# Kernel tuning notes

Hardware: AMD Instinct MI355X
Metric: run time of the kernel (lower is better)

The kernel has to match this reference:

```python
import jax, jax.numpy as jnp
import numpy as np

EMBED_DIM = 1024
NUM_HEADS = 16
HEAD_DIM = EMBED_DIM // NUM_HEADS


def setup_inputs() -> dict:
    key = jax.random.key(0)
    k_x, k_wqkv, k_bqkv, k_wo, k_bo = jax.random.split(key, 5)
    bound = 1.0 / np.sqrt(EMBED_DIM)
    x = jax.random.normal(k_x, (2, 2048, EMBED_DIM), dtype=jnp.float32)
    # torch Linear weight is [out, in]; store as [in, out] for x @ W
    W_qkv = jax.random.uniform(k_wqkv, (EMBED_DIM, 3 * EMBED_DIM), minval=-bound, maxval=bound, dtype=jnp.float32)
    b_qkv = jax.random.uniform(k_bqkv, (3 * EMBED_DIM,), minval=-bound, maxval=bound, dtype=jnp.float32)
    W_out = jax.random.uniform(k_wo, (EMBED_DIM, EMBED_DIM), minval=-bound, maxval=bound, dtype=jnp.float32)
    b_out = jax.random.uniform(k_bo, (EMBED_DIM,), minval=-bound, maxval=bound, dtype=jnp.float32)
    return {"x": x, "W_qkv": W_qkv, "b_qkv": b_qkv, "W_out": W_out, "b_out": b_out}


def reference(x, W_qkv, b_qkv, W_out, b_out):
    B, T, D = x.shape
    H, Hd = NUM_HEADS, HEAD_DIM
    qkv = x @ W_qkv + b_qkv                      # [B,T,3D]
    qkv = qkv.reshape(B, T, 3, H, Hd)
    q = qkv[:, :, 0].transpose(0, 2, 1, 3)       # [B,H,T,Hd]
    k = qkv[:, :, 1].transpose(0, 2, 1, 3)
    v = qkv[:, :, 2].transpose(0, 2, 1, 3)
    scores = jnp.einsum('bhqd,bhkd->bhqk', q, k) / jnp.sqrt(jnp.float32(Hd))
    attn = jax.nn.softmax(scores, axis=-1)       # [B,H,T,T]
    out = jnp.einsum('bhqk,bhkd->bhqd', attn, v) # [B,H,T,Hd]
    out = out.transpose(0, 2, 1, 3).reshape(B, T, D)
    return out @ W_out + b_out
```

## Files before the change

### kernel.cpp

```cpp
#include <hip/hip_runtime.h>
#include <hip/hip_bf16.h>

#define B_   2
#define T_   2048
#define D_   1024
#define H_   16
#define HD_  64
#define M_TOT (B_*T_)
#define N_QKV (3*D_)

typedef __attribute__((ext_vector_type(8))) short bf16x8;
typedef __attribute__((ext_vector_type(4))) float f32x4;
typedef __attribute__((ext_vector_type(16))) float f32x16;

static __device__ __forceinline__ short f2bf(float f) {
    union { __hip_bfloat16 h; short s; } u;
    u.h = __float2bfloat16(f);
    return u.s;
}
static __device__ __forceinline__ unsigned pack2(float a, float b) {
    return (unsigned)(unsigned short)f2bf(a) | ((unsigned)(unsigned short)f2bf(b) << 16);
}
static __device__ __forceinline__ float exp2_fast(float x) {
    return __builtin_amdgcn_exp2f(x);
}
static __device__ __forceinline__ f32x16 zero16() {
    f32x16 z;
    #pragma unroll
    for (int i = 0; i < 16; ++i) z[i] = 0.f;
    return z;
}
static __device__ __forceinline__ void gload16(const void* g, void* l) {
    __builtin_amdgcn_global_load_lds(
        (__attribute__((address_space(1))) unsigned int*)(unsigned long long)g,
        (__attribute__((address_space(3))) unsigned int*)l, 16, 0, 0);
}

__global__ __launch_bounds__(256) void convert_x(const float* __restrict__ x,
                                                 short* __restrict__ xb, int n8) {
    int i = blockIdx.x * blockDim.x + threadIdx.x;
    if (i >= n8) return;
    const float4* p = (const float4*)x + (size_t)i * 2;
    float4 a = p[0], b = p[1];
    bf16x8 o;
    o[0]=f2bf(a.x); o[1]=f2bf(a.y); o[2]=f2bf(a.z); o[3]=f2bf(a.w);
    o[4]=f2bf(b.x); o[5]=f2bf(b.y); o[6]=f2bf(b.z); o[7]=f2bf(b.w);
    *((bf16x8*)xb + i) = o;
}

__global__ __launch_bounds__(256) void transpose_convert(const float* __restrict__ in,
                                                         short* __restrict__ out,
                                                         int K, int N) {
    __shared__ short tile[64][65];
    int k0 = blockIdx.y * 64, n0 = blockIdx.x * 64;
    int t = threadIdx.x;
    #pragma unroll
    for (int i = 0; i < 16; ++i) {
        int idx = i * 256 + t;
        int r = idx >> 6, c = idx & 63;
        tile[r][c] = f2bf(in[(size_t)(k0 + r) * N + n0 + c]);
    }
    __syncthreads();
    #pragma unroll
    for (int i = 0; i < 16; ++i) {
        int idx = i * 256 + t;
        int r = idx >> 6, c = idx & 63;
        out[(size_t)(n0 + r) * K + k0 + c] = tile[c][r];
    }
}

#define QSC 0.18033688f
template<int BM, int BN, int MODE>
__global__ __launch_bounds__(256)
void gemm_dl(const short* __restrict__ A, const short* __restrict__ BT,
             const float* __restrict__ bias, int M, int N, int K,
             short* __restrict__ qo, short* __restrict__ ko,
             short* __restrict__ vo, float* __restrict__ fo) {
    constexpr int BUF = (BM + BN) * 64;
    constexpr int NL = (BM + BN) / 64;
    __shared__ char smem[3 * BUF];
    const int t = threadIdx.x, w = t >> 6, l = t & 63;
    const int qi_l = l & 15, hi_l = l >> 4;
    const int m0 = blockIdx.y * BM, n0 = blockIdx.x * BN;
    const int wr = w >> 1, wc = w & 1;
    constexpr int MI = BM / 32, NI = BN / 32;

    f32x4 acc[MI][NI];
    #pragma unroll
    for (int mi = 0; mi < MI; ++mi)
        #pragma unroll
        for (int ni = 0; ni < NI; ++ni)
            acc[mi][ni] = (f32x4){0.f, 0.f, 0.f, 0.f};

    const int lrow = l >> 2;
    const int lch  = ((l & 3) ^ (lrow & 3)) * 8;

    auto stage = [&](char* dst, int k0) {
        #pragma unroll
        for (int i = 0; i < BM / 64; ++i) {
            int rb = w * (BM / 4) + i * 16;
            gload16(A + (size_t)(m0 + rb + lrow) * K + k0 + lch, dst + rb * 64);
        }
        #pragma unroll
        for (int i = 0; i < BN / 64; ++i) {
            int rb = w * (BN / 4) + i * 16;
            gload16(BT + (size_t)(n0 + rb + lrow) * K + k0 + lch, dst + BM * 64 + rb * 64);
        }
    };

    const int nt = K / 32;
    stage(smem, 0);
    if (nt > 1) stage(smem + BUF, 32);
    for (int it = 0; it < nt; ++it) {
        if (it + 2 < nt) {
            stage(smem + ((it + 2) % 3) * BUF, (it + 2) * 32);
            if constexpr (NL == 4)      asm volatile("s_waitcnt vmcnt(8)" ::: "memory");
            else if constexpr (NL == 3) asm volatile("s_waitcnt vmcnt(6)" ::: "memory");
            else                        asm volatile("s_waitcnt vmcnt(0)" ::: "memory");
        } else if (it + 1 < nt) {
            if constexpr (NL == 4)      asm volatile("s_waitcnt vmcnt(4)" ::: "memory");
            else if constexpr (NL == 3) asm volatile("s_waitcnt vmcnt(3)" ::: "memory");
            else                        asm volatile("s_waitcnt vmcnt(0)" ::: "memory");
        } else {
            asm volatile("s_waitcnt vmcnt(0)" ::: "memory");
        }
        __builtin_amdgcn_s_barrier();

        char* sA = smem + (it % 3) * BUF;
        char* sB = sA + BM * 64;
        bf16x8 af[MI], bfr[NI];
        #pragma unroll
        for (int mi = 0; mi < MI; ++mi) {
            int row = wr * (BM / 2) + mi * 16 + qi_l;
            int ad = row * 64 + ((hi_l ^ (row & 3)) * 16);
            af[mi] = *(const bf16x8*)(sA + ad);
        }
        #pragma unroll
        for (int ni = 0; ni < NI; ++ni) {
            int row = wc * (BN / 2) + ni * 16 + qi_l;
            int ad = row * 64 + ((hi_l ^ (row & 3)) * 16);
            bfr[ni] = *(const bf16x8*)(sB + ad);
        }
        #pragma unroll
        for (int mi = 0; mi < MI; ++mi)
            #pragma unroll
            for (int ni = 0; ni < NI; ++ni)
                acc[mi][ni] = __builtin_amdgcn_mfma_f32_16x16x32_bf16(af[mi], bfr[ni], acc[mi][ni], 0, 0, 0);

        __builtin_amdgcn_s_barrier();
    }

    #pragma unroll
    for (int mi = 0; mi < MI; ++mi) {
        int rbase = m0 + wr * (BM / 2) + mi * 16 + 4 * hi_l;
        #pragma unroll
        for (int ni = 0; ni < NI; ++ni) {
            int n = n0 + wc * (BN / 2) + ni * 16 + qi_l;
            float bv = bias[n];
            #pragma unroll
            for (int r = 0; r < 4; ++r) {
                int mm = rbase + r;
                float c = acc[mi][ni][r] + bv;
                if (MODE == 0) {
                    int which = n >> 10, rest = n & 1023;
                    int h = rest >> 6, d = rest & 63;
                    int b = mm >> 11, tq = mm & 2047;
                    size_t bh = (size_t)(b * H_ + h);
                    if (which == 0)      qo[(bh * T_ + tq) * HD_ + d] = f2bf(c * QSC);
                    else if (which == 1) ko[(bh * T_ + tq) * HD_ + d] = f2bf(c);
                    else                 vo[(bh * HD_ + d) * T_ + tq] = f2bf(c);
                } else {
                    fo[(size_t)mm * N + n] = c;
                }
            }
        }
    }
}

__global__ __launch_bounds__(512)
void attn(const short* __restrict__ q, const short* __restrict__ k,
          const short* __restrict__ vt, short* __restrict__ ao) {
    __shared__ char smem[32768];

    const int t = threadIdx.x, w = t >> 6, l = t & 63;
    const int q32 = l & 31, hi2 = l >> 5;
    const int swz = (l & 7) << 4;
    const int bh = blockIdx.y;
    const int q0 = blockIdx.x * 256 + w * 32;

    const short* qptr = q + ((size_t)bh * T_ + q0) * HD_;
    const short* kbase = k + (size_t)bh * T_ * HD_;
    const short* vbase = vt + (size_t)bh * HD_ * T_;

    const int srow = w * 8 + (l >> 3);
    const int sch  = ((l & 7) ^ (l >> 3)) * 8;

    bf16x8 qa[4];
    #pragma unroll
    for (int kc = 0; kc < 4; ++kc)
        qa[kc] = *(const bf16x8*)(qptr + q32 * HD_ + kc * 16 + hi2 * 8);

    f32x16 o0 = zero16(), o1 = zero16();
    float m = -1e30f, lsum = 0.f;

    gload16(kbase + (size_t)srow * HD_ + sch, smem + srow * 128);
    gload16(vbase + (size_t)srow * T_ + sch,  smem + 8192 + srow * 128);
    __syncthreads();

    int cur = 0;
    for (int kb = 0; kb < T_; kb += 64) {
        char* sK = smem + cur * 16384;
        char* sV = sK + 8192;
        if (kb + 64 < T_) {
            char* nK = smem + (cur ^ 1) * 16384;
            gload16(kbase + (size_t)(kb + 64 + srow) * HD_ + sch, nK + srow * 128);
            gload16(vbase + (size_t)srow * T_ + (kb + 64) + sch,  nK + 8192 + srow * 128);
        }

        f32x16 s0 = zero16(), s1 = zero16();
        #pragma unroll
        for (int kc = 0; kc < 4; ++kc) {
            int off = (kc * 32 + hi2 * 16) ^ swz;
            bf16x8 kf0 = *(const bf16x8*)(sK + q32 * 128 + off);
            s0 = __builtin_amdgcn_mfma_f32_32x32x16_bf16(kf0, qa[kc], s0, 0, 0, 0);
            bf16x8 kf1 = *(const bf16x8*)(sK + (32 + q32) * 128 + off);
            s1 = __builtin_amdgcn_mfma_f32_32x32x16_bf16(kf1, qa[kc], s1, 0, 0, 0);
        }

        float a8[8];
        #pragma unroll
        for (int i = 0; i < 8; ++i)
            a8[i] = fmaxf(fmaxf(s0[i], s0[i + 8]), fmaxf(s1[i], s1[i + 8]));
        float b4_0 = fmaxf(a8[0], a8[1]), b4_1 = fmaxf(a8[2], a8[3]);
        float b4_2 = fmaxf(a8[4], a8[5]), b4_3 = fmaxf(a8[6], a8[7]);
        float tm = fmaxf(fmaxf(b4_0, b4_1), fmaxf(b4_2, b4_3));
        tm = fmaxf(tm, __shfl_xor(tm, 32));

        if (!__all(tm <= m + 8.f)) {
            float mnew = fmaxf(m, tm);
            float fsc = exp2_fast(m - mnew);
            lsum *= fsc;
            #pragma unroll
            for (int i = 0; i < 16; ++i) { o0[i] *= fsc; o1[i] *= fsc; }
            m = mnew;
        }

        #pragma unroll
        for (int i = 0; i < 16; ++i) {
            s0[i] = exp2_fast(s0[i] - m);
            s1[i] = exp2_fast(s1[i] - m);
        }
        float p8[8];
        #pragma unroll
        for (int i = 0; i < 8; ++i)
            p8[i] = (s0[i] + s0[i + 8]) + (s1[i] + s1[i + 8]);
        float psum = ((p8[0] + p8[1]) + (p8[2] + p8[3])) + ((p8[4] + p8[5]) + (p8[6] + p8[7]));
        psum += __shfl_xor(psum, 32);
        lsum += psum;

        unsigned pk0[8], pk1[8];
        #pragma unroll
        for (int p = 0; p < 8; ++p) {
            pk0[p] = pack2(s0[2 * p], s0[2 * p + 1]);
            pk1[p] = pack2(s1[2 * p], s1[2 * p + 1]);
        }

        #pragma unroll
        for (int c = 0; c < 4; ++c) {
            unsigned w0 = (c & 2) ? pk1[(c & 1) * 4 + 0] : pk0[(c & 1) * 4 + 0];
            unsigned w1 = (c & 2) ? pk1[(c & 1) * 4 + 1] : pk0[(c & 1) * 4 + 1];
            unsigned w2 = (c & 2) ? pk1[(c & 1) * 4 + 2] : pk0[(c & 1) * 4 + 2];
            unsigned w3 = (c & 2) ? pk1[(c & 1) * 4 + 3] : pk0[(c & 1) * 4 + 3];
            unsigned t0 = hi2 ? w0 : w2;
            unsigned t1 = hi2 ? w1 : w3;
            unsigned r0 = __shfl_xor(t0, 32);
            unsigned r1 = __shfl_xor(t1, 32);
            union { unsigned u[4]; bf16x8 v; } uf;
            uf.u[0] = hi2 ? r0 : w0;
            uf.u[1] = hi2 ? r1 : w1;
            uf.u[2] = hi2 ? w2 : r0;
            uf.u[3] = hi2 ? w3 : r1;
            bf16x8 pf = uf.v;

            int off = (c * 32 + hi2 * 16) ^ swz;
            bf16x8 vf0 = *(const bf16x8*)(sV + q32 * 128 + off);
            o0 = __builtin_amdgcn_mfma_f32_32x32x16_bf16(vf0, pf, o0, 0, 0, 0);
            bf16x8 vf1 = *(const bf16x8*)(sV + (32 + q32) * 128 + off);
            o1 = __builtin_amdgcn_mfma_f32_32x32x16_bf16(vf1, pf, o1, 0, 0, 0);
        }

        __syncthreads();
        cur ^= 1;
    }

    const float inv = 1.f / lsum;
    const int b = bh >> 4, h = bh & 15;
    const int tq = q0 + q32;
    unsigned* aou = (unsigned*)(ao + ((size_t)(b * T_ + tq)) * D_ + h * HD_);
    #pragma unroll
    for (int pr = 0; pr < 8; ++pr) {
        int d0 = 2 * (pr & 1) + 8 * (pr >> 1) + 4 * hi2;
        aou[d0 >> 1]        = pack2(o0[2 * pr] * inv, o0[2 * pr + 1] * inv);
        aou[(32 + d0) >> 1] = pack2(o1[2 * pr] * inv, o1[2 * pr + 1] * inv);
    }
}

extern "C" void kernel_launch(void* const* d_in, const int* in_sizes, int n_in,
                              void* d_out, int out_size, void* d_ws, size_t ws_size,
                              hipStream_t stream) {
    const float* x    = (const float*)d_in[0];
    const float* Wqkv = (const float*)d_in[1];
    const float* bqkv = (const float*)d_in[2];
    const float* Wout = (const float*)d_in[3];
    const float* bout = (const float*)d_in[4];
    float* out = (float*)d_out;

    char* ws = (char*)d_ws;
    short* xb  = (short*)(ws);
    short* WqT = (short*)(ws + ((size_t)8  << 20));
    short* WoT = (short*)(ws + ((size_t)14 << 20));
    short* qb  = (short*)(ws + ((size_t)16 << 20));
    short* kb  = (short*)(ws + ((size_t)24 << 20));
    short* vtb = (short*)(ws + ((size_t)32 << 20));
    short* aob = (short*)(ws + ((size_t)40 << 20));

    convert_x<<<(M_TOT * D_ / 8 + 255) / 256, 256, 0, stream>>>(x, xb, M_TOT * D_ / 8);
    transpose_convert<<<dim3(N_QKV / 64, D_ / 64), 256, 0, stream>>>(Wqkv, WqT, D_, N_QKV);
    transpose_convert<<<dim3(D_ / 64, D_ / 64), 256, 0, stream>>>(Wout, WoT, D_, D_);

    gemm_dl<128, 128, 0><<<dim3(N_QKV / 128, M_TOT / 128), 256, 0, stream>>>(
        xb, WqT, bqkv, M_TOT, N_QKV, D_, qb, kb, vtb, nullptr);

    attn<<<dim3(T_ / 256, B_ * H_), 512, 0, stream>>>(qb, kb, vtb, aob);

    gemm_dl<128, 64, 1><<<dim3(D_ / 64, M_TOT / 128), 256, 0, stream>>>(
        aob, WoT, bout, M_TOT, D_, D_, nullptr, nullptr, nullptr, out);
}
```

Baseline: 130.3 us.

## Split attention KV range in two and merge partials with combine kernel

```diff
diff --git a/kernel.cpp b/kernel.cpp
--- a/kernel.cpp
+++ b/kernel.cpp
@@ -17,6 +17,11 @@
     union { __hip_bfloat16 h; short s; } u;
     u.h = __float2bfloat16(f);
     return u.s;
+}
+static __device__ __forceinline__ float bf2f(short s) {
+    union { unsigned u; float f; } v;
+    v.u = ((unsigned)(unsigned short)s) << 16;
+    return v.f;
 }
 static __device__ __forceinline__ unsigned pack2(float a, float b) {
     return (unsigned)(unsigned short)f2bf(a) | ((unsigned)(unsigned short)f2bf(b) << 16);
@@ -179,14 +184,17 @@
 
 __global__ __launch_bounds__(512)
 void attn(const short* __restrict__ q, const short* __restrict__ k,
-          const short* __restrict__ vt, short* __restrict__ ao) {
+          const short* __restrict__ vt, short* __restrict__ pO,
+          float2* __restrict__ ml) {
     __shared__ char smem[32768];
 
     const int t = threadIdx.x, w = t >> 6, l = t & 63;
     const int q32 = l & 31, hi2 = l >> 5;
     const int swz = (l & 7) << 4;
     const int bh = blockIdx.y;
+    const int sp = blockIdx.z;
     const int q0 = blockIdx.x * 256 + w * 32;
+    const int kv0 = sp * (T_ / 2);
 
     const short* qptr = q + ((size_t)bh * T_ + q0) * HD_;
     const short* kbase = k + (size_t)bh * T_ * HD_;
@@ -203,18 +211,18 @@
     f32x16 o0 = zero16(), o1 = zero16();
     float m = -1e30f, lsum = 0.f;
 
-    gload16(kbase + (size_t)srow * HD_ + sch, smem + srow * 128);
-    gload16(vbase + (size_t)srow * T_ + sch,  smem + 8192 + srow * 128);
+    gload16(kbase + (size_t)(kv0 + srow) * HD_ + sch, smem + srow * 128);
+    gload16(vbase + (size_t)srow * T_ + kv0 + sch,    smem + 8192 + srow * 128);
     __syncthreads();
 
     int cur = 0;
-    for (int kb = 0; kb < T_; kb += 64) {
+    for (int kb = 0; kb < T_ / 2; kb += 64) {
         char* sK = smem + cur * 16384;
         char* sV = sK + 8192;
-        if (kb + 64 < T_) {
+        if (kb + 64 < T_ / 2) {
             char* nK = smem + (cur ^ 1) * 16384;
-            gload16(kbase + (size_t)(kb + 64 + srow) * HD_ + sch, nK + srow * 128);
-            gload16(vbase + (size_t)srow * T_ + (kb + 64) + sch,  nK + 8192 + srow * 128);
+            gload16(kbase + (size_t)(kv0 + kb + 64 + srow) * HD_ + sch, nK + srow * 128);
+            gload16(vbase + (size_t)srow * T_ + kv0 + kb + 64 + sch,   nK + 8192 + srow * 128);
         }
 
         f32x16 s0 = zero16(), s1 = zero16();
@@ -294,15 +302,44 @@
     }
 
     const float inv = 1.f / lsum;
-    const int b = bh >> 4, h = bh & 15;
     const int tq = q0 + q32;
-    unsigned* aou = (unsigned*)(ao + ((size_t)(b * T_ + tq)) * D_ + h * HD_);
+    size_t prow = ((size_t)sp * 32 + bh) * T_ + tq;
+    unsigned* pou = (unsigned*)(pO + prow * 64);
     #pragma unroll
     for (int pr = 0; pr < 8; ++pr) {
         int d0 = 2 * (pr & 1) + 8 * (pr >> 1) + 4 * hi2;
-        aou[d0 >> 1]        = pack2(o0[2 * pr] * inv, o0[2 * pr + 1] * inv);
-        aou[(32 + d0) >> 1] = pack2(o1[2 * pr] * inv, o1[2 * pr + 1] * inv);
-    }
+        pou[d0 >> 1]        = pack2(o0[2 * pr] * inv, o0[2 * pr + 1] * inv);
+        pou[(32 + d0) >> 1] = pack2(o1[2 * pr] * inv, o1[2 * pr + 1] * inv);
+    }
+    if (hi2 == 0) ml[prow] = make_float2(m, lsum);
+}
+
+__global__ __launch_bounds__(256)
+void combine(const short* __restrict__ pO, const float2* __restrict__ ml,
+             short* __restrict__ aob) {
+    int idx = blockIdx.x * 256 + threadIdx.x;
+    int e0 = idx * 8;
+    int row = e0 >> 6;
+    int dc = e0 & 63;
+    const int SPOFF = 32 * T_;
+
+    float2 ml0 = ml[row], ml1 = ml[row + SPOFF];
+    float M = fmaxf(ml0.x, ml1.x);
+    float w0 = ml0.y * exp2_fast(ml0.x - M);
+    float w1 = ml1.y * exp2_fast(ml1.x - M);
+    float inv = 1.f / (w0 + w1);
+    w0 *= inv; w1 *= inv;
+
+    bf16x8 r0 = ((const bf16x8*)pO)[idx];
+    bf16x8 r1 = ((const bf16x8*)pO)[idx + SPOFF * 8];
+    bf16x8 o;
+    #pragma unroll
+    for (int j = 0; j < 8; ++j)
+        o[j] = f2bf(w0 * bf2f(r0[j]) + w1 * bf2f(r1[j]));
+
+    int bh = row >> 11, tq = row & 2047;
+    int b = bh >> 4, h = bh & 15;
+    *(bf16x8*)(aob + ((size_t)(b * T_ + tq)) * D_ + h * HD_ + dc) = o;
 }
 
 extern "C" void kernel_launch(void* const* d_in, const int* in_sizes, int n_in,
@@ -318,11 +355,13 @@
     char* ws = (char*)d_ws;
     short* xb  = (short*)(ws);
     short* WqT = (short*)(ws + ((size_t)8  << 20));
-    short* WoT = (short*)(ws + ((size_t)14 << 20));
     short* qb  = (short*)(ws + ((size_t)16 << 20));
     short* kb  = (short*)(ws + ((size_t)24 << 20));
     short* vtb = (short*)(ws + ((size_t)32 << 20));
     short* aob = (short*)(ws + ((size_t)40 << 20));
+    short* WoT = (short*)(ws + ((size_t)48 << 20));
+    float2* mlp = (float2*)(ws + ((size_t)50 << 20));
+    short*  pO = (short*)(ws);
 
     convert_x<<<(M_TOT * D_ / 8 + 255) / 256, 256, 0, stream>>>(x, xb, M_TOT * D_ / 8);
     transpose_convert<<<dim3(N_QKV / 64, D_ / 64), 256, 0, stream>>>(Wqkv, WqT, D_, N_QKV);
@@ -331,7 +370,8 @@
     gemm_dl<128, 128, 0><<<dim3(N_QKV / 128, M_TOT / 128), 256, 0, stream>>>(
         xb, WqT, bqkv, M_TOT, N_QKV, D_, qb, kb, vtb, nullptr);
 
-    attn<<<dim3(T_ / 256, B_ * H_), 512, 0, stream>>>(qb, kb, vtb, aob);
+    attn<<<dim3(T_ / 256, B_ * H_, 2), 512, 0, stream>>>(qb, kb, vtb, pO, mlp);
+    combine<<<(M_TOT * D_ / 8) / 256, 256, 0, stream>>>(pO, mlp, aob);
 
     gemm_dl<128, 64, 1><<<dim3(D_ / 64, M_TOT / 128), 256, 0, stream>>>(
         aob, WoT, bout, M_TOT, D_, D_, nullptr, nullptr, nullptr, out);
```

Result: slower. 136.2 us (+4.5%).
